# Kernel tuning notes

Measured on AMD Instinct MI355X. Metric: run time of the kernel, lower is better.

Reference implementation:

```python
import jax, jax.numpy as jnp
import numpy as np


def setup_inputs() -> dict:
    key = jax.random.key(0)
    k1, k2, k3, k4 = jax.random.split(key, 4)
    B, Cin, Cout, N, modes = 16, 128, 128, 8192, 64
    scale = 1.0 / (Cin * Cout)
    x = jax.random.normal(k1, (B, Cin, N), dtype=jnp.float32)
    # spectral weight: [in, out, modes, 2] uniform in [0, scale) like torch.rand * scale
    w_spec = scale * jax.random.uniform(k2, (Cin, Cout, modes, 2), dtype=jnp.float32)
    # Conv1d(kernel=1) weight [out, in] and bias [out] (kaiming-uniform-ish init)
    bound = 1.0 / np.sqrt(Cin)
    w_conv = jax.random.uniform(k3, (Cout, Cin), minval=-bound, maxval=bound, dtype=jnp.float32)
    b_conv = jax.random.uniform(k4, (Cout,), minval=-bound, maxval=bound, dtype=jnp.float32)
    return {"x": x, "w_spec": w_spec, "w_conv": w_conv, "b_conv": b_conv}


def reference(x, w_spec, w_conv, b_conv):
    N = x.shape[-1]
    modes = w_spec.shape[2]
    n_freq = N // 2 + 1
    # Spectral conv: rfft, keep first `modes` coefficients, complex channel mix
    x_ft = jnp.fft.rfft(x)  # [B, Cin, n_freq] complex64
    w_c = w_spec[..., 0] + 1j * w_spec[..., 1]  # [Cin, Cout, modes]
    out_m = jnp.einsum('bim,iom->bom', x_ft[:, :, :modes], w_c)  # [B, Cout, modes]
    out_ft = jnp.pad(out_m, ((0, 0), (0, 0), (0, n_freq - modes)))
    x1 = jnp.fft.irfft(out_ft, n=N)  # [B, Cout, N]
    # 1x1 conv (pointwise channel mix)
    x2 = jnp.einsum('bin,oi->bon', x, w_conv) + b_conv[None, :, None]
    return jax.nn.gelu(x1 + x2, approximate=False)
```

## Files before the change

kernel.cpp:

```cpp
#include <hip/hip_runtime.h>
#include <hip/hip_bf16.h>
#include <math.h>

#define NB    16
#define NCIN  128
#define NCOUT 128
#define NN    8192
#define NMOD  64

typedef short bf16x8 __attribute__((ext_vector_type(8)));
typedef float f32x4  __attribute__((ext_vector_type(4)));

#define MFMA16(a, b, c) __builtin_amdgcn_mfma_f32_16x16x32_bf16((a), (b), (c), 0, 0, 0)

__device__ inline unsigned short f2bf_rne(float f) {
    unsigned u = __float_as_uint(f);
    u += 0x7FFF + ((u >> 16) & 1);
    return (unsigned short)(u >> 16);
}
__device__ inline short f2bf_trunc(float f) {
    return (short)(__float_as_uint(f) >> 16);
}

__global__ __launch_bounds__(256) void k_prep(const float* __restrict__ wc,
                                              const float* __restrict__ wsp,
                                              unsigned short* __restrict__ T,
                                              unsigned short* __restrict__ Tt,
                                              unsigned short* __restrict__ Wcb,
                                              unsigned short* __restrict__ Wpk) {
    const float C = 7.66990393943e-4f;
    if (blockIdx.x < 16) {
        int a = blockIdx.x * 256 + threadIdx.x;
        int k = a >> 6, n0 = (a & 63) * 128;
        for (int j8 = 0; j8 < 16; ++j8) {
            short c8[8], s8[8];
            #pragma unroll
            for (int j = 0; j < 8; ++j) {
                int n = n0 + j8 * 8 + j;
                int ph = (k * n) & (NN - 1);
                float sn, cs; __sincosf((float)ph * C, &sn, &cs);
                c8[j] = (short)f2bf_rne(cs);
                s8[j] = (short)f2bf_rne(-sn);
            }
            *(bf16x8*)(T + (size_t)(2 * k) * NN + n0 + j8 * 8)     = *(bf16x8*)c8;
            *(bf16x8*)(T + (size_t)(2 * k + 1) * NN + n0 + j8 * 8) = *(bf16x8*)s8;
        }
    } else if (blockIdx.x < 48) {
        int n = (blockIdx.x - 16) * 256 + threadIdx.x;
        for (int k4 = 0; k4 < 16; ++k4) {
            short buf[8];
            #pragma unroll
            for (int j = 0; j < 4; ++j) {
                int k = k4 * 4 + j;
                int ph = (n * k) & (NN - 1);
                float sn, cs; __sincosf((float)ph * C, &sn, &cs);
                buf[2 * j]     = (short)f2bf_rne(cs);
                buf[2 * j + 1] = (short)f2bf_rne(-sn);
            }
            *(bf16x8*)(Tt + (size_t)n * 128 + k4 * 8) = *(bf16x8*)buf;
        }
    } else if (blockIdx.x < 112) {
        int j = (blockIdx.x - 48) * 256 + threadIdx.x;
        if (j < NCOUT * NCIN) Wcb[j] = f2bf_rne(wc[j]);
    } else {
        int o = blockIdx.x - 112;
        __shared__ float2 wl[8192];
        {
            int i = threadIdx.x >> 1, h2 = threadIdx.x & 1;
            const float2* src = (const float2*)wsp + (size_t)(i * 128 + o) * 64 + h2 * 32;
            float2* dst = wl + i * 64 + h2 * 32;
            #pragma unroll
            for (int j = 0; j < 32; j += 4) {
                float4 v0 = *(const float4*)(src + j);
                float4 v1 = *(const float4*)(src + j + 2);
                *(float4*)(dst + j)     = v0;
                *(float4*)(dst + j + 2) = v1;
            }
        }
        __syncthreads();
        int k = threadIdx.x >> 2, qc = threadIdx.x & 3;
        const float s = (k == 0) ? (1.f / NN) : (2.f / NN);
        unsigned short* wre = Wpk + ((size_t)(k * 2 + 0) * 128 + o) * 256 + qc * 64;
        unsigned short* wim = wre + 32768;
        #pragma unroll
        for (int c8 = 0; c8 < 4; ++c8) {
            short re16[16], im16[16];
            #pragma unroll
            for (int t = 0; t < 8; ++t) {
                int i = qc * 32 + c8 * 8 + t;
                float2 wv = wl[i * 64 + k];
                float wr = s * wv.x, wi = s * wv.y;
                re16[2 * t]     = (short)f2bf_rne(wr);
                re16[2 * t + 1] = (short)f2bf_rne(-wi);
                im16[2 * t]     = (k == 0) ? (short)0 : (short)f2bf_rne(wi);
                im16[2 * t + 1] = (k == 0) ? (short)0 : (short)f2bf_rne(wr);
            }
            *(bf16x8*)(wre + c8 * 16)     = *(bf16x8*)re16;
            *(bf16x8*)(wre + c8 * 16 + 8) = *(bf16x8*)(re16 + 8);
            *(bf16x8*)(wim + c8 * 16)     = *(bf16x8*)im16;
            *(bf16x8*)(wim + c8 * 16 + 8) = *(bf16x8*)(im16 + 8);
        }
    }
}

__global__ __launch_bounds__(256) void k_dftmm(const float* __restrict__ x,
                                               const unsigned short* __restrict__ T,
                                               float* __restrict__ Cpart) {
    const int mt = blockIdx.x & 63, sp = blockIdx.x >> 6;
    const int w = threadIdx.x >> 6, l = threadIdx.x & 63;
    const int l15 = l & 15, q = l >> 4;
    const int colbase = w * 32;
    __shared__ short As[8192];

    const int sr = threadIdx.x >> 3;
    const int sc = threadIdx.x & 7;
    const float* xrow = x + (size_t)(mt * 32 + sr) * NN + sp * 512 + sc * 16;
    short* wp0 = As + sr * 128 + (((sc * 2    ) ^ (sr & 7)) * 8);
    short* wp1 = As + sr * 128 + (((sc * 2 + 1) ^ (sr & 7)) * 8);

    float4 ra, rb, rc, rd;
#define LOADC(c) { const float* p_ = xrow + (c) * 128;                         \
        ra = *(const float4*)p_;       rb = *(const float4*)(p_ + 4);          \
        rc = *(const float4*)(p_ + 8); rd = *(const float4*)(p_ + 12); }
#define WRITEC(bufi) {                                                          \
        short t0_[8] = { f2bf_trunc(ra.x), f2bf_trunc(ra.y), f2bf_trunc(ra.z), f2bf_trunc(ra.w), \
                         f2bf_trunc(rb.x), f2bf_trunc(rb.y), f2bf_trunc(rb.z), f2bf_trunc(rb.w) }; \
        short t1_[8] = { f2bf_trunc(rc.x), f2bf_trunc(rc.y), f2bf_trunc(rc.z), f2bf_trunc(rc.w), \
                         f2bf_trunc(rd.x), f2bf_trunc(rd.y), f2bf_trunc(rd.z), f2bf_trunc(rd.w) }; \
        *(bf16x8*)(wp0 + (bufi) * 4096) = *(bf16x8*)t0_;                        \
        *(bf16x8*)(wp1 + (bufi) * 4096) = *(bf16x8*)t1_; }

    const unsigned short* Tp0 = T + (size_t)(colbase + l15) * NN + sp * 512 + q * 8;
    const unsigned short* Tp1 = Tp0 + (size_t)16 * NN;

    const int rsw = l15 & 7;

    LOADC(0);
    WRITEC(0);
    __syncthreads();

    f32x4 acc[2][2] = {};
    int buf = 0;
    for (int c = 0; c < 4; ++c) {
        if (c < 3) LOADC(c + 1);
        const short* Ab = As + buf * 4096;
        #pragma unroll
        for (int kk = 0; kk < 4; ++kk) {
            int ce = ((kk * 4 + q) ^ rsw) * 8;
            bf16x8 a0 = *(const bf16x8*)(Ab + l15 * 128 + ce);
            bf16x8 a1 = *(const bf16x8*)(Ab + (16 + l15) * 128 + ce);
            bf16x8 b0 = *(const bf16x8*)(Tp0 + c * 128 + kk * 32);
            bf16x8 b1 = *(const bf16x8*)(Tp1 + c * 128 + kk * 32);
            acc[0][0] = MFMA16(a0, b0, acc[0][0]);
            acc[0][1] = MFMA16(a0, b1, acc[0][1]);
            acc[1][0] = MFMA16(a1, b0, acc[1][0]);
            acc[1][1] = MFMA16(a1, b1, acc[1][1]);
        }
        if (c < 3) {
            WRITEC(buf ^ 1);
            __syncthreads();
            buf ^= 1;
        }
    }
#undef LOADC
#undef WRITEC

    #pragma unroll
    for (int mf = 0; mf < 2; ++mf)
        #pragma unroll
        for (int nf = 0; nf < 2; ++nf) {
            int col  = colbase + nf * 16 + l15;
            int row0 = mt * 32 + mf * 16 + q * 4;
            *(f32x4*)(Cpart + (size_t)sp * 262144 + (size_t)col * 2048 + row0) = acc[mf][nf];
        }
}

__global__ __launch_bounds__(256) void k_reduce(const float* __restrict__ Cpart,
                                                unsigned short* __restrict__ Axh) {
    int t = blockIdx.x * 256 + threadIdx.x;
    float s = 0.f;
    #pragma unroll
    for (int sp = 0; sp < 16; ++sp) s += Cpart[(size_t)sp * 262144 + t];
    int col = t >> 11, row = t & 2047;
    int k = col >> 1, p = col & 1;
    int b = row >> 7, i = row & 127;
    Axh[((size_t)k * 16 + b) * 256 + i * 2 + p] = f2bf_rne(s);
}

__global__ __launch_bounds__(64) void k_mixmm(const unsigned short* __restrict__ Axh,
                                              const unsigned short* __restrict__ Wpk,
                                              unsigned short* __restrict__ Aspec) {
    const int k = blockIdx.x >> 3, oq = blockIdx.x & 7;
    const int l = threadIdx.x, l15 = l & 15, q = l >> 4;
    f32x4 ar = {}, ai = {};
    const unsigned short* Ab = Axh + ((size_t)k * 16 + l15) * 256;
    const int o = oq * 16 + l15;
    #pragma unroll
    for (int kt = 0; kt < 8; ++kt) {
        bf16x8 a = *(const bf16x8*)(Ab + kt * 32 + q * 8);
        const unsigned short* wb = Wpk + ((size_t)(k * 2) * 128 + o) * 256 + kt * 32 + q * 8;
        bf16x8 bre = *(const bf16x8*)wb;
        bf16x8 bim = *(const bf16x8*)(wb + 32768);
        ar = MFMA16(a, bre, ar);
        ai = MFMA16(a, bim, ai);
    }
    #pragma unroll
    for (int r = 0; r < 4; ++r) {
        int b = q * 4 + r;
        unsigned v = (unsigned)f2bf_rne(ar[r]) | ((unsigned)f2bf_rne(ai[r]) << 16);
        *(unsigned*)(Aspec + ((size_t)b * 128 + o) * 128 + 2 * k) = v;
    }
}

__global__ __launch_bounds__(256) void k_out(const float* __restrict__ x,
                                             const unsigned short* __restrict__ Tt,
                                             const unsigned short* __restrict__ Aspec,
                                             const unsigned short* __restrict__ Wcb,
                                             const float* __restrict__ bias,
                                             float* __restrict__ out) {
    const int b = blockIdx.x >> 7, nt = blockIdx.x & 127;
    const int w = threadIdx.x >> 6, l = threadIdx.x & 63;
    const int l15 = l & 15, q = l >> 4;
    const int wo = w >> 1, wn = w & 1;
    __shared__ short xs[8192];

    const float* xb = x + (size_t)b * 128 * NN + nt * 64;
    #pragma unroll
    for (int it = 0; it < 4; ++it) {
        int unit = it * 256 + threadIdx.x;
        int ipair = unit >> 4, nq = unit & 15;
        int i0 = ipair * 2;
        const float* p0 = xb + (size_t)i0 * NN + nq * 4;
        float4 r0 = *(const float4*)p0;
        float4 r1 = *(const float4*)(p0 + NN);
        float a0[4] = { r0.x, r0.y, r0.z, r0.w };
        float a1[4] = { r1.x, r1.y, r1.z, r1.w };
        #pragma unroll
        for (int j = 0; j < 4; ++j) {
            int n = nq * 4 + j;
            unsigned v = (unsigned)(unsigned short)f2bf_trunc(a0[j])
                       | ((unsigned)(unsigned short)f2bf_trunc(a1[j]) << 16);
            int swz = (n ^ (n >> 2)) & 15;
            int addr = n * 128 + (((i0 >> 3) ^ swz) * 8) + (i0 & 7);
            *(unsigned*)&xs[addr] = v;
        }
    }

    const int obase = wo * 64;
    const int nbase = nt * 64 + wn * 32;
    f32x4 acc[4][2] = {};
    #pragma unroll
    for (int kt = 0; kt < 4; ++kt) {
        bf16x8 bb[2];
        #pragma unroll
        for (int nf = 0; nf < 2; ++nf) {
            int n = nbase + nf * 16 + l15;
            bb[nf] = *(const bf16x8*)(Tt + (size_t)n * 128 + kt * 32 + q * 8);
        }
        const unsigned short* Ap = Aspec + (size_t)b * 16384 + kt * 32 + q * 8;
        #pragma unroll
        for (int mf = 0; mf < 4; ++mf) {
            bf16x8 a = *(const bf16x8*)(Ap + (size_t)(obase + mf * 16 + l15) * 128);
            acc[mf][0] = MFMA16(a, bb[0], acc[mf][0]);
            acc[mf][1] = MFMA16(a, bb[1], acc[mf][1]);
        }
    }
    __syncthreads();
    #pragma unroll
    for (int kt = 0; kt < 4; ++kt) {
        bf16x8 bb[2];
        #pragma unroll
        for (int nf = 0; nf < 2; ++nf) {
            int nl = wn * 32 + nf * 16 + l15;
            int c  = kt * 4 + q;
            int swz = (nl ^ (nl >> 2)) & 15;
            bb[nf] = *(const bf16x8*)&xs[nl * 128 + ((c ^ swz) * 8)];
        }
        const unsigned short* Ap = Wcb + kt * 32 + q * 8;
        #pragma unroll
        for (int mf = 0; mf < 4; ++mf) {
            bf16x8 a = *(const bf16x8*)(Ap + (size_t)(obase + mf * 16 + l15) * 128);
            acc[mf][0] = MFMA16(a, bb[0], acc[mf][0]);
            acc[mf][1] = MFMA16(a, bb[1], acc[mf][1]);
        }
    }
    #pragma unroll
    for (int mf = 0; mf < 4; ++mf)
        #pragma unroll
        for (int nf = 0; nf < 2; ++nf)
            #pragma unroll
            for (int r = 0; r < 4; ++r) {
                int o = obase + mf * 16 + q * 4 + r;
                int n = nbase + nf * 16 + l15;
                float v = acc[mf][nf][r] + bias[o];
                float u = v * v;
                float p = v * fmaf(0.0713548162f, u, 1.5957691216f);
                float e = __expf(-p);
                float g = v * __builtin_amdgcn_rcpf(1.f + e);
                out[((size_t)(b * 128 + o)) * NN + n] = g;
            }
}

extern "C" void kernel_launch(void* const* d_in, const int* in_sizes, int n_in,
                              void* d_out, int out_size, void* d_ws, size_t ws_size,
                              hipStream_t stream) {
    const float* x    = (const float*)d_in[0];
    const float* wsp  = (const float*)d_in[1];
    const float* wc   = (const float*)d_in[2];
    const float* bc   = (const float*)d_in[3];
    float* out = (float*)d_out;

    unsigned short* T   = (unsigned short*)d_ws;
    unsigned short* Tt  = T + (size_t)1048576;
    unsigned short* Wcb = Tt + (size_t)1048576;
    unsigned short* Asp = Wcb + 16384;
    unsigned short* Wpk = Asp + 262144;
    float* Cpart = (float*)(Wpk + (size_t)8388608);
    unsigned short* Axh = (unsigned short*)(Cpart + (size_t)16 * 262144);

    k_prep  <<<240,  256, 0, stream>>>(wc, wsp, T, Tt, Wcb, Wpk);
    k_dftmm <<<1024, 256, 0, stream>>>(x, T, Cpart);
    k_reduce<<<1024, 256, 0, stream>>>(Cpart, Axh);
    k_mixmm <<<512,  64,  0, stream>>>(Axh, Wpk, Asp);
    k_out   <<<2048, 256, 0, stream>>>(x, Tt, Asp, Wcb, bc, out);
}
```

Measured before the change: 191.4 us.

## Split prep kernel and double DFT GEMM row tile to reuse twiddle loads

The forward DFT GEMM now gives each block 64 rows of x instead of 32. Each global load of twiddle B fragments then feeds twice as many MFMAs, and the grid halves to 512 blocks. The prep kernel is split into a trig-table kernel and a weight-packing kernel, and the T-table generation is spread over 64 blocks instead of 16 so it runs with more parallelism. The larger tile doubles LDS use and accumulator registers, which may reduce occupancy.

```diff
diff --git a/kernel.cpp b/kernel.cpp
--- a/kernel.cpp
+++ b/kernel.cpp
@@ -22,17 +22,14 @@
     return (short)(__float_as_uint(f) >> 16);
 }
 
-__global__ __launch_bounds__(256) void k_prep(const float* __restrict__ wc,
-                                              const float* __restrict__ wsp,
-                                              unsigned short* __restrict__ T,
-                                              unsigned short* __restrict__ Tt,
-                                              unsigned short* __restrict__ Wcb,
-                                              unsigned short* __restrict__ Wpk) {
+__global__ __launch_bounds__(256) void k_trig(unsigned short* __restrict__ T,
+                                              unsigned short* __restrict__ Tt) {
     const float C = 7.66990393943e-4f;
-    if (blockIdx.x < 16) {
+    if (blockIdx.x < 64) {
         int a = blockIdx.x * 256 + threadIdx.x;
-        int k = a >> 6, n0 = (a & 63) * 128;
-        for (int j8 = 0; j8 < 16; ++j8) {
+        int k = a >> 8, n0 = (a & 255) * 32;
+        #pragma unroll
+        for (int j8 = 0; j8 < 4; ++j8) {
             short c8[8], s8[8];
             #pragma unroll
             for (int j = 0; j < 8; ++j) {
@@ -45,8 +42,8 @@
             *(bf16x8*)(T + (size_t)(2 * k) * NN + n0 + j8 * 8)     = *(bf16x8*)c8;
             *(bf16x8*)(T + (size_t)(2 * k + 1) * NN + n0 + j8 * 8) = *(bf16x8*)s8;
         }
-    } else if (blockIdx.x < 48) {
-        int n = (blockIdx.x - 16) * 256 + threadIdx.x;
+    } else {
+        int n = (blockIdx.x - 64) * 256 + threadIdx.x;
         for (int k4 = 0; k4 < 16; ++k4) {
             short buf[8];
             #pragma unroll
@@ -59,11 +56,15 @@
             }
             *(bf16x8*)(Tt + (size_t)n * 128 + k4 * 8) = *(bf16x8*)buf;
         }
-    } else if (blockIdx.x < 112) {
-        int j = (blockIdx.x - 48) * 256 + threadIdx.x;
-        if (j < NCOUT * NCIN) Wcb[j] = f2bf_rne(wc[j]);
-    } else {
-        int o = blockIdx.x - 112;
+    }
+}
+
+__global__ __launch_bounds__(256) void k_wpk(const float* __restrict__ wc,
+                                             const float* __restrict__ wsp,
+                                             unsigned short* __restrict__ Wcb,
+                                             unsigned short* __restrict__ Wpk) {
+    if (blockIdx.x < 128) {
+        int o = blockIdx.x;
         __shared__ float2 wl[8192];
         {
             int i = threadIdx.x >> 1, h2 = threadIdx.x & 1;
@@ -100,35 +101,41 @@
             *(bf16x8*)(wim + c8 * 16)     = *(bf16x8*)im16;
             *(bf16x8*)(wim + c8 * 16 + 8) = *(bf16x8*)(im16 + 8);
         }
+    } else {
+        int j = (blockIdx.x - 128) * 256 + threadIdx.x;
+        if (j < NCOUT * NCIN) Wcb[j] = f2bf_rne(wc[j]);
     }
 }
 
 __global__ __launch_bounds__(256) void k_dftmm(const float* __restrict__ x,
                                                const unsigned short* __restrict__ T,
                                                float* __restrict__ Cpart) {
-    const int mt = blockIdx.x & 63, sp = blockIdx.x >> 6;
+    const int mt = blockIdx.x & 31, sp = blockIdx.x >> 5;
     const int w = threadIdx.x >> 6, l = threadIdx.x & 63;
     const int l15 = l & 15, q = l >> 4;
     const int colbase = w * 32;
-    __shared__ short As[8192];
-
-    const int sr = threadIdx.x >> 3;
-    const int sc = threadIdx.x & 7;
-    const float* xrow = x + (size_t)(mt * 32 + sr) * NN + sp * 512 + sc * 16;
-    short* wp0 = As + sr * 128 + (((sc * 2    ) ^ (sr & 7)) * 8);
-    short* wp1 = As + sr * 128 + (((sc * 2 + 1) ^ (sr & 7)) * 8);
-
-    float4 ra, rb, rc, rd;
-#define LOADC(c) { const float* p_ = xrow + (c) * 128;                         \
-        ra = *(const float4*)p_;       rb = *(const float4*)(p_ + 4);          \
-        rc = *(const float4*)(p_ + 8); rd = *(const float4*)(p_ + 12); }
+    __shared__ short As[16384];
+
+    const int sr = threadIdx.x >> 2;
+    const int sc = threadIdx.x & 3;
+    const float* xrow = x + (size_t)(mt * 64 + sr) * NN + sp * 512 + sc * 32;
+    short* wbase = As + sr * 128;
+
+    float4 r0_, r1_, r2_, r3_, r4_, r5_, r6_, r7_;
+#define LOADC(c) { const float* p_ = xrow + (c) * 128;                          \
+        r0_ = *(const float4*)p_;        r1_ = *(const float4*)(p_ + 4);        \
+        r2_ = *(const float4*)(p_ + 8);  r3_ = *(const float4*)(p_ + 12);       \
+        r4_ = *(const float4*)(p_ + 16); r5_ = *(const float4*)(p_ + 20);       \
+        r6_ = *(const float4*)(p_ + 24); r7_ = *(const float4*)(p_ + 28); }
+#define PACK2(dst, u, v) { short t_[8] = {                                      \
+        f2bf_trunc(u.x), f2bf_trunc(u.y), f2bf_trunc(u.z), f2bf_trunc(u.w),     \
+        f2bf_trunc(v.x), f2bf_trunc(v.y), f2bf_trunc(v.z), f2bf_trunc(v.w) };   \
+        *(bf16x8*)(dst) = *(bf16x8*)t_; }
 #define WRITEC(bufi) {                                                          \
-        short t0_[8] = { f2bf_trunc(ra.x), f2bf_trunc(ra.y), f2bf_trunc(ra.z), f2bf_trunc(ra.w), \
-                         f2bf_trunc(rb.x), f2bf_trunc(rb.y), f2bf_trunc(rb.z), f2bf_trunc(rb.w) }; \
-        short t1_[8] = { f2bf_trunc(rc.x), f2bf_trunc(rc.y), f2bf_trunc(rc.z), f2bf_trunc(rc.w), \
-                         f2bf_trunc(rd.x), f2bf_trunc(rd.y), f2bf_trunc(rd.z), f2bf_trunc(rd.w) }; \
-        *(bf16x8*)(wp0 + (bufi) * 4096) = *(bf16x8*)t0_;                        \
-        *(bf16x8*)(wp1 + (bufi) * 4096) = *(bf16x8*)t1_; }
+        PACK2(wbase + (bufi)*8192 + (((sc*4+0) ^ (sr&7))*8), r0_, r1_);         \
+        PACK2(wbase + (bufi)*8192 + (((sc*4+1) ^ (sr&7))*8), r2_, r3_);         \
+        PACK2(wbase + (bufi)*8192 + (((sc*4+2) ^ (sr&7))*8), r4_, r5_);         \
+        PACK2(wbase + (bufi)*8192 + (((sc*4+3) ^ (sr&7))*8), r6_, r7_); }
 
     const unsigned short* Tp0 = T + (size_t)(colbase + l15) * NN + sp * 512 + q * 8;
     const unsigned short* Tp1 = Tp0 + (size_t)16 * NN;
@@ -139,22 +146,22 @@
     WRITEC(0);
     __syncthreads();
 
-    f32x4 acc[2][2] = {};
+    f32x4 acc[4][2] = {};
     int buf = 0;
     for (int c = 0; c < 4; ++c) {
         if (c < 3) LOADC(c + 1);
-        const short* Ab = As + buf * 4096;
+        const short* Ab = As + buf * 8192;
         #pragma unroll
         for (int kk = 0; kk < 4; ++kk) {
             int ce = ((kk * 4 + q) ^ rsw) * 8;
-            bf16x8 a0 = *(const bf16x8*)(Ab + l15 * 128 + ce);
-            bf16x8 a1 = *(const bf16x8*)(Ab + (16 + l15) * 128 + ce);
             bf16x8 b0 = *(const bf16x8*)(Tp0 + c * 128 + kk * 32);
             bf16x8 b1 = *(const bf16x8*)(Tp1 + c * 128 + kk * 32);
-            acc[0][0] = MFMA16(a0, b0, acc[0][0]);
-            acc[0][1] = MFMA16(a0, b1, acc[0][1]);
-            acc[1][0] = MFMA16(a1, b0, acc[1][0]);
-            acc[1][1] = MFMA16(a1, b1, acc[1][1]);
+            #pragma unroll
+            for (int mf = 0; mf < 4; ++mf) {
+                bf16x8 a = *(const bf16x8*)(Ab + (mf * 16 + l15) * 128 + ce);
+                acc[mf][0] = MFMA16(a, b0, acc[mf][0]);
+                acc[mf][1] = MFMA16(a, b1, acc[mf][1]);
+            }
         }
         if (c < 3) {
             WRITEC(buf ^ 1);
@@ -163,14 +170,15 @@
         }
     }
 #undef LOADC
+#undef PACK2
 #undef WRITEC
 
     #pragma unroll
-    for (int mf = 0; mf < 2; ++mf)
+    for (int mf = 0; mf < 4; ++mf)
         #pragma unroll
         for (int nf = 0; nf < 2; ++nf) {
             int col  = colbase + nf * 16 + l15;
-            int row0 = mt * 32 + mf * 16 + q * 4;
+            int row0 = mt * 64 + mf * 16 + q * 4;
             *(f32x4*)(Cpart + (size_t)sp * 262144 + (size_t)col * 2048 + row0) = acc[mf][nf];
         }
 }
@@ -318,8 +326,9 @@
     float* Cpart = (float*)(Wpk + (size_t)8388608);
     unsigned short* Axh = (unsigned short*)(Cpart + (size_t)16 * 262144);
 
-    k_prep  <<<240,  256, 0, stream>>>(wc, wsp, T, Tt, Wcb, Wpk);
-    k_dftmm <<<1024, 256, 0, stream>>>(x, T, Cpart);
+    k_trig  <<<96,   256, 0, stream>>>(T, Tt);
+    k_wpk   <<<192,  256, 0, stream>>>(wc, wsp, Wcb, Wpk);
+    k_dftmm <<<512,  256, 0, stream>>>(x, T, Cpart);
     k_reduce<<<1024, 256, 0, stream>>>(Cpart, Axh);
     k_mixmm <<<512,  64,  0, stream>>>(Axh, Wpk, Asp);
     k_out   <<<2048, 256, 0, stream>>>(x, Tt, Asp, Wcb, bc, out);
```

Result: no change. 188.7 us (-1.4%).
